# Kernel optimization log

Measured on AMD Instinct MI355X. Metric: run time of the kernel, lower is better.

The kernel has to match this reference:

```python
import jax, jax.numpy as jnp
import numpy as np

VOCAB, D, S, W, B = 32000, 768, 512, 300, 64
LMAX = 4  # max chars per word (spans are 1-3 chars)


def setup_inputs() -> dict:
    key = jax.random.key(0)
    k1, k2, k3, k4 = jax.random.split(key, 4)
    ernie_output = jax.random.normal(k1, (B, S, D), dtype=jnp.float32)
    word_embedding = jax.random.normal(k2, (VOCAB, D), dtype=jnp.float32)
    # structured word_index: (word_id, char_start, char_end) with contiguous spans
    lengths = jax.random.randint(k3, (B, W), 1, LMAX)  # 1..3 chars per word
    starts = 1 + jnp.concatenate(
        [jnp.zeros((B, 1), jnp.int32), jnp.cumsum(lengths, axis=1)[:, :-1]], axis=1
    ).astype(jnp.int32)
    ends = starts + lengths.astype(jnp.int32)  # tail words exceed S -> fallback path
    word_ids = jax.random.randint(k4, (B, W), 0, VOCAB, dtype=jnp.int32)
    word_index = jnp.stack([word_ids, starts, ends], axis=-1)  # (B, W, 3)
    return {"ernie_output": ernie_output, "word_embedding": word_embedding,
            "word_index": word_index}


def reference(ernie_output, word_embedding, word_index):
    Bb, Ss, Dd = ernie_output.shape
    Ww = word_index.shape[1]
    wid = word_index[..., 0]    # (B, W)
    st = word_index[..., 1]
    en = word_index[..., 2]
    span = en - st

    we = word_embedding[wid]                        # (B, W, D) query / fallback emb
    pos = st[..., None] + jnp.arange(LMAX)          # (B, W, LMAX)
    pos_c = jnp.clip(pos, 0, Ss - 1)
    chars = ernie_output[jnp.arange(Bb)[:, None, None], pos_c]  # (B, W, LMAX, D)

    # masked softmax attention pooling over the char span (len==1 reduces to copy)
    mask = jnp.arange(LMAX)[None, None, :] < jnp.maximum(span, 1)[..., None]
    scores = jnp.einsum('bwd,bwld->bwl', we, chars)
    scores = jnp.where(mask, scores, -jnp.inf)
    attn = jax.nn.softmax(scores, axis=-1)
    pooled = jnp.einsum('bwl,bwld->bwd', attn, chars)  # (B, W, D)

    in_range = en < Ss
    normal = jnp.where(in_range[..., None], pooled, we)

    # break semantics: first word with end<S and span<=0 fills positions j.. with
    # that word's embedding
    brk = in_range & (span <= 0)                   # (B, W)
    has_brk = jnp.any(brk, axis=1)
    first = jnp.where(has_brk, jnp.argmax(brk, axis=1), Ww)  # (B,)
    fill_id = wid[jnp.arange(Bb), jnp.clip(first, 0, Ww - 1)]
    fill = word_embedding[fill_id]                 # (B, D)
    jidx = jnp.arange(Ww)[None, :]
    out = jnp.where((jidx >= first[:, None])[..., None], fill[:, None, :], normal)
    return out
```

## Files before the change

kernel.cpp:

```cpp
#include <hip/hip_runtime.h>
#include <math.h>

#define VOCAB 32000
#define D 768
#define S 512
#define W 300
#define B 64
#define LMAX 4

typedef float f32x4 __attribute__((ext_vector_type(4)));

__global__ __launch_bounds__(64) void find_first_kernel(
    const int* __restrict__ word_index,
    int* __restrict__ first_out,
    int* __restrict__ fill_id_out)
{
    const int b = blockIdx.x;
    const int lane = threadIdx.x;
    int my_first = W;
    for (int w = lane; w < W; w += 64) {
        const int base = (b * W + w) * 3;
        const int st = word_index[base + 1];
        const int en = word_index[base + 2];
        if (en < S && (en - st) <= 0) my_first = min(my_first, w);
    }
    #pragma unroll
    for (int off = 32; off > 0; off >>= 1)
        my_first = min(my_first, __shfl_xor(my_first, off));
    if (lane == 0) {
        first_out[b] = my_first;
        const int fw = min(my_first, W - 1);
        fill_id_out[b] = word_index[(b * W + fw) * 3 + 0];
    }
}

__device__ __forceinline__ float wave_bcast_sum(float p) {
    #pragma unroll
    for (int off = 32; off > 0; off >>= 1) p += __shfl_xor(p, off);
    return p;
}

__global__ __launch_bounds__(256) void pool_kernel(
    const float* __restrict__ ernie,
    const float* __restrict__ emb,
    const int*   __restrict__ word_index,
    const int*   __restrict__ first_arr,
    const int*   __restrict__ fill_arr,
    float* __restrict__ out)
{
    int gwave = (int)((blockIdx.x * blockDim.x + threadIdx.x) >> 6);
    gwave = __builtin_amdgcn_readfirstlane(gwave);
    const int lane = threadIdx.x & 63;

    const int b = gwave / W;
    const int w = gwave - b * W;

    const int base = gwave * 3;
    const int wid = word_index[base + 0];
    const int st  = word_index[base + 1];
    const int en  = word_index[base + 2];

    f32x4* __restrict__ outp = (f32x4*)(out + (size_t)gwave * D);

    if (w >= first_arr[b]) {
        const f32x4* src = (const f32x4*)(emb + (size_t)fill_arr[b] * D);
        #pragma unroll
        for (int k = 0; k < 3; k++)
            __builtin_nontemporal_store(src[lane + 64 * k], &outp[lane + 64 * k]);
        return;
    }

    const f32x4* wep = (const f32x4*)(emb + (size_t)wid * D);
    f32x4 we0 = wep[lane], we1 = wep[lane + 64], we2 = wep[lane + 128];

    if (en >= S) {
        __builtin_nontemporal_store(we0, &outp[lane]);
        __builtin_nontemporal_store(we1, &outp[lane + 64]);
        __builtin_nontemporal_store(we2, &outp[lane + 128]);
        return;
    }

    const int span_eff = min(max(en - st, 1), LMAX);
    const f32x4* erow = (const f32x4*)(ernie + (size_t)b * S * D);

    float m = -INFINITY, denom = 0.f;
    f32x4 acc0 = 0.f, acc1 = 0.f, acc2 = 0.f;

    int p0 = min(max(st, 0), S - 1);
    f32x4 c0 = erow[p0 * 192 + lane];
    f32x4 c1 = erow[p0 * 192 + lane + 64];
    f32x4 c2 = erow[p0 * 192 + lane + 128];

    #pragma unroll
    for (int l = 0; l < LMAX; ++l) {
        if (l >= span_eff) break;
        f32x4 n0, n1, n2;
        if (l + 1 < span_eff) {
            int pn = min(max(st + l + 1, 0), S - 1);
            n0 = erow[pn * 192 + lane];
            n1 = erow[pn * 192 + lane + 64];
            n2 = erow[pn * 192 + lane + 128];
        } else {
            n0 = c0; n1 = c1; n2 = c2;
        }
        f32x4 pv = c0 * we0 + c1 * we1 + c2 * we2;
        float p = pv.x + pv.y + pv.z + pv.w;
        p = wave_bcast_sum(p);
        float mn = fmaxf(m, p);
        float scale = expf(m - mn);
        float e = expf(p - mn);
        denom = denom * scale + e;
        acc0 = acc0 * scale + e * c0;
        acc1 = acc1 * scale + e * c1;
        acc2 = acc2 * scale + e * c2;
        m = mn;
        c0 = n0; c1 = n1; c2 = n2;
    }

    const float inv = 1.f / denom;
    __builtin_nontemporal_store(acc0 * inv, &outp[lane]);
    __builtin_nontemporal_store(acc1 * inv, &outp[lane + 64]);
    __builtin_nontemporal_store(acc2 * inv, &outp[lane + 128]);
}

extern "C" void kernel_launch(void* const* d_in, const int* in_sizes, int n_in,
                              void* d_out, int out_size, void* d_ws, size_t ws_size,
                              hipStream_t stream) {
    const float* ernie      = (const float*)d_in[0];
    const float* emb        = (const float*)d_in[1];
    const int*   word_index = (const int*)d_in[2];
    float* out = (float*)d_out;

    int* first_arr = (int*)d_ws;
    int* fill_arr  = first_arr + B;

    find_first_kernel<<<B, 64, 0, stream>>>(word_index, first_arr, fill_arr);

    const int total_waves = B * W;
    const int grid = total_waves / 4;
    pool_kernel<<<grid, 256, 0, stream>>>(ernie, emb, word_index,
                                          first_arr, fill_arr, out);
}
```

Measured before the change: 227.1 us.

## Stage shared char rows in LDS via async global-to-LDS loads per word group

Each 256-thread block now handles four consecutive words of one batch row. It copies the contiguous span of ernie rows they cover (up to 12 rows) into shared memory with global_load_lds, then each wave reads its char rows from LDS. Before, each wave loaded its own rows from global memory, so the aim is to cut redundant global traffic and per-wave load latency. The fill and fallback paths are merged into one embedding load. The cost is 36KB of LDS per block, which limits occupancy, plus a block-wide barrier that all waves wait on, including early-exit ones.

```diff
diff --git a/kernel.cpp b/kernel.cpp
--- a/kernel.cpp
+++ b/kernel.cpp
@@ -7,6 +7,10 @@
 #define W 300
 #define B 64
 #define LMAX 4
+#define GW 4
+#define WGPB 75
+#define MAXROWS 12
+#define ROWB 3072
 
 typedef float f32x4 __attribute__((ext_vector_type(4)));
 
@@ -40,6 +44,13 @@
     return p;
 }
 
+__device__ __forceinline__ void async_copy16(const void* g, void* l) {
+    __builtin_amdgcn_global_load_lds(
+        (const __attribute__((address_space(1))) void*)g,
+        (__attribute__((address_space(3))) void*)l,
+        16, 0, 0);
+}
+
 __global__ __launch_bounds__(256) void pool_kernel(
     const float* __restrict__ ernie,
     const float* __restrict__ emb,
@@ -48,32 +59,42 @@
     const int*   __restrict__ fill_arr,
     float* __restrict__ out)
 {
-    int gwave = (int)((blockIdx.x * blockDim.x + threadIdx.x) >> 6);
-    gwave = __builtin_amdgcn_readfirstlane(gwave);
-    const int lane = threadIdx.x & 63;
+    __shared__ __align__(16) char smem[MAXROWS * ROWB];
 
-    const int b = gwave / W;
-    const int w = gwave - b * W;
+    const int blk = blockIdx.x;
+    const int b   = blk / WGPB;
+    const int wg  = blk - b * WGPB;
+    const int w0  = wg * GW;
+    const int lane   = threadIdx.x & 63;
+    const int waveid = __builtin_amdgcn_readfirstlane(threadIdx.x >> 6);
+    const int w      = w0 + waveid;
+    const int gwave  = b * W + w;
 
-    const int base = gwave * 3;
-    const int wid = word_index[base + 0];
-    const int st  = word_index[base + 1];
-    const int en  = word_index[base + 2];
+    const int st0 = word_index[(b * W + w0) * 3 + 1];
+    const int en3 = word_index[(b * W + w0 + GW - 1) * 3 + 2];
+    int row_lo = max(min(st0, S), 0);
+    int row_hi = min(en3, S);
+    int nrows  = min(max(row_hi - row_lo, 0), MAXROWS);
+
+    const int wid = word_index[gwave * 3 + 0];
+    const int st  = word_index[gwave * 3 + 1];
+    const int en  = word_index[gwave * 3 + 2];
+    const int first = first_arr[b];
+    const int rowid = (w >= first) ? fill_arr[b] : wid;
+
+    const f32x4* wep = (const f32x4*)(emb + (size_t)rowid * D);
+    f32x4 we0 = wep[lane], we1 = wep[lane + 64], we2 = wep[lane + 128];
+
+    const char* gbase = (const char*)(ernie + ((size_t)b * S + row_lo) * D);
+    const int nchunk = nrows * 3;
+    for (int c = waveid; c < nchunk; c += 4)
+        async_copy16(gbase + c * 1024 + lane * 16, smem + c * 1024);
+
+    __syncthreads();
 
     f32x4* __restrict__ outp = (f32x4*)(out + (size_t)gwave * D);
 
-    if (w >= first_arr[b]) {
-        const f32x4* src = (const f32x4*)(emb + (size_t)fill_arr[b] * D);
-        #pragma unroll
-        for (int k = 0; k < 3; k++)
-            __builtin_nontemporal_store(src[lane + 64 * k], &outp[lane + 64 * k]);
-        return;
-    }
-
-    const f32x4* wep = (const f32x4*)(emb + (size_t)wid * D);
-    f32x4 we0 = wep[lane], we1 = wep[lane + 64], we2 = wep[lane + 128];
-
-    if (en >= S) {
+    if (w >= first || en >= S) {
         __builtin_nontemporal_store(we0, &outp[lane]);
         __builtin_nontemporal_store(we1, &outp[lane + 64]);
         __builtin_nontemporal_store(we2, &outp[lane + 128]);
@@ -81,28 +102,18 @@
     }
 
     const int span_eff = min(max(en - st, 1), LMAX);
-    const f32x4* erow = (const f32x4*)(ernie + (size_t)b * S * D);
+    const char* lbase = smem + (size_t)(st - row_lo) * ROWB;
 
     float m = -INFINITY, denom = 0.f;
     f32x4 acc0 = 0.f, acc1 = 0.f, acc2 = 0.f;
 
-    int p0 = min(max(st, 0), S - 1);
-    f32x4 c0 = erow[p0 * 192 + lane];
-    f32x4 c1 = erow[p0 * 192 + lane + 64];
-    f32x4 c2 = erow[p0 * 192 + lane + 128];
-
     #pragma unroll
     for (int l = 0; l < LMAX; ++l) {
         if (l >= span_eff) break;
-        f32x4 n0, n1, n2;
-        if (l + 1 < span_eff) {
-            int pn = min(max(st + l + 1, 0), S - 1);
-            n0 = erow[pn * 192 + lane];
-            n1 = erow[pn * 192 + lane + 64];
-            n2 = erow[pn * 192 + lane + 128];
-        } else {
-            n0 = c0; n1 = c1; n2 = c2;
-        }
+        const f32x4* cp = (const f32x4*)(lbase + l * ROWB);
+        f32x4 c0 = cp[lane];
+        f32x4 c1 = cp[lane + 64];
+        f32x4 c2 = cp[lane + 128];
         f32x4 pv = c0 * we0 + c1 * we1 + c2 * we2;
         float p = pv.x + pv.y + pv.z + pv.w;
         p = wave_bcast_sum(p);
@@ -114,7 +125,6 @@
         acc1 = acc1 * scale + e * c1;
         acc2 = acc2 * scale + e * c2;
         m = mn;
-        c0 = n0; c1 = n1; c2 = n2;
     }
 
     const float inv = 1.f / denom;
@@ -136,8 +146,7 @@
 
     find_first_kernel<<<B, 64, 0, stream>>>(word_index, first_arr, fill_arr);
 
-    const int total_waves = B * W;
-    const int grid = total_waves / 4;
+    const int grid = B * WGPB;
     pool_kernel<<<grid, 256, 0, stream>>>(ernie, emb, word_index,
                                           first_arr, fill_arr, out);
 }
```

Measured after the change: 228.9 us. Within noise of the previous version (+0.8%).
